# Performance work log

Hardware: AMD Instinct MI355X
Metric: run time of the kernel (lower is better)

The kernel has to match this reference:

```python
import jax, jax.numpy as jnp
import numpy as np

N = 50000
IN_CH = 128
HID = 32
HEADS = 4
OUT_CH = 64
NEG_SLOPE = 0.2


def glorot(key, shape):
    fan = shape[0] + shape[-1] if len(shape) > 1 else shape[0]
    s = jnp.sqrt(6.0 / fan)
    return jax.random.uniform(key, shape, jnp.float32, -s, s)


def setup_inputs() -> dict:
    key = jax.random.key(0)
    ks = jax.random.split(key, 10)
    x = jax.random.normal(ks[0], (N, IN_CH), jnp.float32)
    edge_index = jax.random.randint(ks[1], (2, 800000), 0, N, jnp.int32)
    return {
        "x": x,
        "edge_index": edge_index,
        # layer 1 (heads=4, concat)
        "W1": glorot(ks[2], (IN_CH, HEADS * HID)),
        "att_src1": glorot(ks[3], (HEADS, HID)),
        "att_dst1": glorot(ks[4], (HEADS, HID)),
        "b1": jnp.zeros((HEADS * HID,), jnp.float32),
        # layer 2 (heads=1, no concat)
        "W2": glorot(ks[5], (HEADS * HID, OUT_CH)),
        "att_src2": glorot(ks[6], (1, OUT_CH)),
        "att_dst2": glorot(ks[7], (1, OUT_CH)),
        "b2": jnp.zeros((OUT_CH,), jnp.float32),
    }


def gat_conv(x, src, dst, W, att_src, att_dst, b, heads, out_ch, concat):
    n = x.shape[0]
    h = (x @ W).reshape(n, heads, out_ch)                  # [N,H,C]
    a_s = jnp.einsum("nhc,hc->nh", h, att_src)            # [N,H]
    a_d = jnp.einsum("nhc,hc->nh", h, att_dst)            # [N,H]
    e = jax.nn.leaky_relu(a_s[src] + a_d[dst], NEG_SLOPE)  # [E,H]
    # segment softmax over incoming edges of each destination node
    m = jax.ops.segment_max(e, dst, num_segments=n)
    ex = jnp.exp(e - m[dst])
    denom = jax.ops.segment_sum(ex, dst, num_segments=n)
    alpha = ex / (denom[dst] + 1e-16)                      # [E,H]
    msg = h[src] * alpha[:, :, None]                       # [E,H,C]
    out = jax.ops.segment_sum(msg, dst, num_segments=n)    # [N,H,C]
    out = out.reshape(n, heads * out_ch) if concat else out.mean(axis=1)
    return out + b


def _forward(x, edge_index, W1, att_src1, att_dst1, b1, W2, att_src2, att_dst2, b2):
    n = x.shape[0]
    loop = jnp.arange(n, dtype=edge_index.dtype)
    src = jnp.concatenate([edge_index[0], loop])  # PyG adds self-loops
    dst = jnp.concatenate([edge_index[1], loop])
    h = gat_conv(x, src, dst, W1, att_src1, att_dst1, b1, HEADS, HID, True)
    h = jax.nn.relu(h)
    return gat_conv(h, src, dst, W2, att_src2, att_dst2, b2, 1, OUT_CH, False)


def reference(x, edge_index, W1, att_src1, att_dst1, b1, W2, att_src2, att_dst2, b2):
    return _forward(x, edge_index, W1, att_src1, att_dst1, b1, W2, att_src2, att_dst2, b2)
```

## Files before the change

kernel.cpp:

```cpp
#include <hip/hip_runtime.h>

#define NEG_SLOPE 0.2f

typedef unsigned int uint32;
typedef unsigned short ushort;
typedef unsigned long long u64;
typedef __fp16 f16x2 __attribute__((ext_vector_type(2)));
typedef __fp16 half8 __attribute__((ext_vector_type(8)));
typedef float f32x4 __attribute__((ext_vector_type(4)));

constexpr int IN_CH = 128;
constexpr int HID = 32;
constexpr int HEADS = 4;
constexpr int OUT_CH = 64;
constexpr int C1 = HEADS * HID;
constexpr int RB = 1024;

__device__ inline uint32 pk_f16(float lo, float hi) {
    f16x2 h = __builtin_amdgcn_cvt_pkrtz(lo, hi);
    uint32 r;
    __builtin_memcpy(&r, &h, 4);
    return r;
}
__device__ inline float f16_lo(uint32 v) {
    f16x2 h;
    __builtin_memcpy(&h, &v, 4);
    return (float)h[0];
}
__device__ inline float f16_hi(uint32 v) {
    f16x2 h;
    __builtin_memcpy(&h, &v, 4);
    return (float)h[1];
}
__device__ inline float leaky(float e) {
    return fmaxf(e, 0.f) + NEG_SLOPE * fminf(e, 0.f);
}


__global__ __launch_bounds__(256) void pack_hist_kernel(const int* __restrict__ ei, int E,
                                                        uint32* __restrict__ packed,
                                                        int* __restrict__ gcount) {
    __shared__ int lh[256];
    int t = threadIdx.x;
    lh[t] = 0;
    __syncthreads();
    int base0 = blockIdx.x * RB;
#pragma unroll
    for (int j = 0; j < 4; j++) {
        int e = base0 + j * 256 + t;
        if (e < E) {
            uint32 s = (uint32)ei[e], d = (uint32)ei[E + e];
            uint32 v = (d << 16) | s;
            packed[e] = v;
            atomicAdd(&lh[v >> 24], 1);
        }
    }
    __syncthreads();
    if (lh[t]) atomicAdd(&gcount[t], lh[t]);
}

__global__ __launch_bounds__(256) void bases_kernel(const int* __restrict__ gcount,
                                                    int* __restrict__ gbase,
                                                    int* __restrict__ cursor, int E) {
    __shared__ int cum[256];
    int t = threadIdx.x;
    int v = gcount[t];
    cum[t] = v;
    __syncthreads();
    for (int d = 1; d < 256; d <<= 1) {
        int x = (t >= d) ? cum[t - d] : 0;
        __syncthreads();
        cum[t] += x;
        __syncthreads();
    }
    int excl = cum[t] - v;
    gbase[t] = excl;
    cursor[t] = excl;
    if (t == 255) gbase[256] = E;
}

__global__ __launch_bounds__(256) void scatter_msd_kernel(const uint32* __restrict__ in,
                                                          uint32* __restrict__ out,
                                                          int* __restrict__ cursor, int E) {
    __shared__ int lcnt[256];
    __shared__ int lbase[256];
    int t = threadIdx.x;
    lcnt[t] = 0;
    __syncthreads();
    int base0 = blockIdx.x * RB;
    uint32 vals[4];
    int bks[4], rank[4];
    bool val[4];
#pragma unroll
    for (int j = 0; j < 4; j++) {
        int e = base0 + j * 256 + t;
        val[j] = e < E;
        uint32 v = val[j] ? in[e] : 0u;
        vals[j] = v;
        int b = v >> 24;
        bks[j] = b;
        if (val[j]) rank[j] = atomicAdd(&lcnt[b], 1);
    }
    __syncthreads();
    if (lcnt[t] > 0) lbase[t] = atomicAdd(&cursor[t], lcnt[t]);
    __syncthreads();
#pragma unroll
    for (int j = 0; j < 4; j++)
        if (val[j]) out[lbase[bks[j]] + rank[j]] = vals[j];
}

__global__ __launch_bounds__(256) void local_sort_kernel(const uint32* __restrict__ in,
                                                         uint32* __restrict__ out,
                                                         const int* __restrict__ gbase,
                                                         int* __restrict__ offsets, int N, int E) {
    __shared__ int hist[256];
    __shared__ int cum[256];
    int b = blockIdx.x;
    int t = threadIdx.x;
    int segstart = gbase[b];
    int segend = gbase[b + 1];
    hist[t] = 0;
    __syncthreads();
    for (int i = segstart + t; i < segend; i += 256) atomicAdd(&hist[(in[i] >> 16) & 0xff], 1);
    __syncthreads();
    int v = hist[t];
    cum[t] = v;
    __syncthreads();
    for (int d = 1; d < 256; d <<= 1) {
        int x = (t >= d) ? cum[t - d] : 0;
        __syncthreads();
        cum[t] += x;
        __syncthreads();
    }
    int myExcl = cum[t] - v;
    int dstv = b * 256 + t;
    if (dstv < N) offsets[dstv] = segstart + myExcl;
    if (b == 0 && t == 0) offsets[N] = E;
    hist[t] = myExcl;
    __syncthreads();
    for (int i = segstart + t; i < segend; i += 256) {
        uint32 w = in[i];
        int slot = atomicAdd(&hist[(w >> 16) & 0xff], 1);
        out[segstart + slot] = w;
    }
}


template <int K, int COLS, int H, bool AF16>
__global__ __launch_bounds__(256) void gemm_dots_kernel(
    const float* __restrict__ A, const float* __restrict__ W,
    const float* __restrict__ att_s, const float* __restrict__ att_d,
    uint32* __restrict__ hb, float* __restrict__ as_, float* __restrict__ ad_, int N) {
    static_assert(K == 128, "");
    constexpr int CF = COLS / 16;
    __shared__ ushort xs[64][136];
    __shared__ ushort wt[COLS][136];
    int tid = threadIdx.x;
    int row0 = blockIdx.x * 64;

#pragma unroll
    for (int l = 0; l < 4; l++) {
        int idx = tid + l * 256;
        int row = idx >> 4, kc = idx & 15;
        uint4 pkv = make_uint4(0, 0, 0, 0);
        if (row0 + row < N) {
            if constexpr (AF16) {
                pkv = *(const uint4*)((const uint32*)A + (size_t)(row0 + row) * (K / 2) + kc * 4);
            } else {
                const float* ap = A + (size_t)(row0 + row) * K + kc * 8;
                float4 v0 = *(const float4*)ap;
                float4 v1 = *(const float4*)(ap + 4);
                pkv = make_uint4(pk_f16(v0.x, v0.y), pk_f16(v0.z, v0.w), pk_f16(v1.x, v1.y),
                                 pk_f16(v1.z, v1.w));
            }
        }
        *(uint4*)&xs[row][kc * 8] = pkv;
    }
    constexpr int NP = (K / 2) * COLS / 256;
#pragma unroll
    for (int l = 0; l < NP; l++) {
        int p = tid + l * 256;
        int col = p % COLS, kp = p / COLS;
        float v0 = W[(size_t)(2 * kp) * COLS + col];
        float v1 = W[(size_t)(2 * kp + 1) * COLS + col];
        *(uint32*)&wt[col][kp * 2] = pk_f16(v0, v1);
    }
    __syncthreads();

    int w = tid >> 6, l = tid & 63;
    int q = l & 15, g = l >> 4;

    half8 af[4];
#pragma unroll
    for (int ks = 0; ks < 4; ks++) af[ks] = *(const half8*)&xs[w * 16 + q][ks * 32 + g * 8];

    f32x4 accs[CF];
#pragma unroll
    for (int cf = 0; cf < CF; cf++) {
        f32x4 a = {0.f, 0.f, 0.f, 0.f};
#pragma unroll
        for (int ks = 0; ks < 4; ks++) {
            half8 bf = *(const half8*)&wt[cf * 16 + q][ks * 32 + g * 8];
            a = __builtin_amdgcn_mfma_f32_16x16x32_f16(af[ks], bf, a, 0, 0, 0);
        }
        accs[cf] = a;
    }

    float asf[CF], adf[CF];
#pragma unroll
    for (int cf = 0; cf < CF; cf++) {
        asf[cf] = att_s[cf * 16 + q];
        adf[cf] = att_d[cf * 16 + q];
    }

#pragma unroll
    for (int r = 0; r < 4; r++) {
        int n_r = row0 + w * 16 + g * 4 + r;
        uint32 dw[CF];
        float p0 = 0.f, p1 = 0.f, p2 = 0.f, p3 = 0.f;
        float d0 = 0.f, d1 = 0.f, d2 = 0.f, d3 = 0.f;
#pragma unroll
        for (int cf = 0; cf < CF; cf++) {
            float v = accs[cf][r];
            float nb = __shfl_xor(v, 1);
            float ev = (q & 1) ? nb : v;
            float ov = (q & 1) ? v : nb;
            dw[cf] = pk_f16(ev, ov);
            float cs = v * asf[cf], cd = v * adf[cf];
            if constexpr (H == 4) {
                if (cf < 2) {
                    p0 += cs;
                    d0 += cd;
                } else if (cf < 4) {
                    p1 += cs;
                    d1 += cd;
                } else if (cf < 6) {
                    p2 += cs;
                    d2 += cd;
                } else {
                    p3 += cs;
                    d3 += cd;
                }
            } else {
                p0 += cs;
                d0 += cd;
            }
        }
#pragma unroll
        for (int dd = 1; dd < 16; dd <<= 1) {
            p0 += __shfl_xor(p0, dd);
            d0 += __shfl_xor(d0, dd);
            if constexpr (H == 4) {
                p1 += __shfl_xor(p1, dd);
                d1 += __shfl_xor(d1, dd);
                p2 += __shfl_xor(p2, dd);
                d2 += __shfl_xor(d2, dd);
                p3 += __shfl_xor(p3, dd);
                d3 += __shfl_xor(d3, dd);
            }
        }
        if (n_r < N) {
            if ((q & 1) == 0) {
                uint32* hp = hb + (size_t)n_r * (COLS / 2) + (q >> 1);
#pragma unroll
                for (int cf = 0; cf < CF; cf++) hp[cf * 8] = dw[cf];
            }
            if constexpr (H == 4) {
                if ((q >> 2) == r) {
                    int hh = q & 3;
                    float vs = hh == 0 ? p0 : hh == 1 ? p1 : hh == 2 ? p2 : p3;
                    float vd = hh == 0 ? d0 : hh == 1 ? d1 : hh == 2 ? d2 : d3;
                    as_[(size_t)n_r * 4 + hh] = vs;
                    ad_[(size_t)n_r * 4 + hh] = vd;
                }
            } else {
                if (q == r) {
                    as_[n_r] = p0;
                    ad_[n_r] = d0;
                }
            }
        }
    }
}


template <int C, int H, bool RELU, bool OUTF16>
__global__ __launch_bounds__(256) void aggregate_kernel(
    const uint32* __restrict__ hb, const float* __restrict__ as_,
    const float* __restrict__ ad_, const int* __restrict__ offsets,
    const uint32* __restrict__ csr, const float* __restrict__ bias, void* __restrict__ outp,
    int N) {
    __shared__ float plds[4][64 * H];
    __shared__ int slds[4][64];
    int gid = blockIdx.x * blockDim.x + threadIdx.x;
    int n = gid >> 6;
    int lane = threadIdx.x & 63;
    int wslot = threadIdx.x >> 6;
    if (n >= N) return;
    int off = offsets[n];
    int deg = offsets[n + 1] - off;

    float ad[H], s[H];
#pragma unroll
    for (int h = 0; h < H; h++) {
        ad[h] = ad_[(size_t)n * H + h];
        s[h] = 0.f;
    }

    constexpr int G = C / 8;
    constexpr int EPI = 64 / G;
    int eg = lane / G;
    int cl = lane % G;
    int hsel = (H == 4) ? (cl >> 2) : 0;
    float acc[8];
#pragma unroll
    for (int j = 0; j < 8; j++) acc[j] = 0.f;

    for (int base = 0; base <= deg; base += 64) {
        int my = base + lane;
        int cnt = min(64, deg + 1 - base);
        if (my <= deg) {
            int si = (my < deg) ? (int)(csr[off + my] & 0xffffu) : n;
            slds[wslot][lane] = si;
            if constexpr (H == 4) {
                float4 a = ((const float4*)as_)[si];
                float q0 = __expf(fminf(leaky(a.x + ad[0]), 80.f));
                float q1 = __expf(fminf(leaky(a.y + ad[1]), 80.f));
                float q2 = __expf(fminf(leaky(a.z + ad[2]), 80.f));
                float q3 = __expf(fminf(leaky(a.w + ad[3]), 80.f));
                s[0] += q0;
                s[1] += q1;
                s[2] += q2;
                s[3] += q3;
                ((float4*)plds[wslot])[lane] = make_float4(q0, q1, q2, q3);
            } else {
                float p = __expf(fminf(leaky(as_[si] + ad[0]), 80.f));
                s[0] += p;
                plds[wslot][lane] = p;
            }
        }
        int t2 = 0;
        for (; t2 + 2 * EPI <= cnt; t2 += 2 * EPI) {
            int tA = t2 + eg, tB = t2 + EPI + eg;
            int srcA = slds[wslot][tA];
            int srcB = slds[wslot][tB];
            float alA = plds[wslot][tA * H + hsel];
            float alB = plds[wslot][tB * H + hsel];
            uint4 uA = *(const uint4*)(hb + (size_t)srcA * (C / 2) + cl * 4);
            uint4 uB = *(const uint4*)(hb + (size_t)srcB * (C / 2) + cl * 4);
            acc[0] = fmaf(alA, f16_lo(uA.x), acc[0]);
            acc[1] = fmaf(alA, f16_hi(uA.x), acc[1]);
            acc[2] = fmaf(alA, f16_lo(uA.y), acc[2]);
            acc[3] = fmaf(alA, f16_hi(uA.y), acc[3]);
            acc[4] = fmaf(alA, f16_lo(uA.z), acc[4]);
            acc[5] = fmaf(alA, f16_hi(uA.z), acc[5]);
            acc[6] = fmaf(alA, f16_lo(uA.w), acc[6]);
            acc[7] = fmaf(alA, f16_hi(uA.w), acc[7]);
            acc[0] = fmaf(alB, f16_lo(uB.x), acc[0]);
            acc[1] = fmaf(alB, f16_hi(uB.x), acc[1]);
            acc[2] = fmaf(alB, f16_lo(uB.y), acc[2]);
            acc[3] = fmaf(alB, f16_hi(uB.y), acc[3]);
            acc[4] = fmaf(alB, f16_lo(uB.z), acc[4]);
            acc[5] = fmaf(alB, f16_hi(uB.z), acc[5]);
            acc[6] = fmaf(alB, f16_lo(uB.w), acc[6]);
            acc[7] = fmaf(alB, f16_hi(uB.w), acc[7]);
        }
        for (; t2 < cnt; t2 += EPI) {
            int te = t2 + eg;
            bool valid = te < cnt;
            int tc = valid ? te : 0;
            int src = slds[wslot][tc];
            float al = plds[wslot][tc * H + hsel];
            al = valid ? al : 0.f;
            uint4 u = *(const uint4*)(hb + (size_t)src * (C / 2) + cl * 4);
            acc[0] = fmaf(al, f16_lo(u.x), acc[0]);
            acc[1] = fmaf(al, f16_hi(u.x), acc[1]);
            acc[2] = fmaf(al, f16_lo(u.y), acc[2]);
            acc[3] = fmaf(al, f16_hi(u.y), acc[3]);
            acc[4] = fmaf(al, f16_lo(u.z), acc[4]);
            acc[5] = fmaf(al, f16_hi(u.z), acc[5]);
            acc[6] = fmaf(al, f16_lo(u.w), acc[6]);
            acc[7] = fmaf(al, f16_hi(u.w), acc[7]);
        }
    }

#pragma unroll
    for (int d = 1; d < 64; d <<= 1)
#pragma unroll
        for (int h = 0; h < H; h++) s[h] += __shfl_xor(s[h], d);
#pragma unroll
    for (int d = G; d < 64; d <<= 1)
#pragma unroll
        for (int j = 0; j < 8; j++) acc[j] += __shfl_xor(acc[j], d);

    if (eg == 0) {
        float inv = 1.f / s[hsel];
        int c = cl * 8;
        float o[8];
#pragma unroll
        for (int j = 0; j < 8; j++) {
            o[j] = fmaf(acc[j], inv, bias[c + j]);
            if (RELU) o[j] = fmaxf(o[j], 0.f);
        }
        if constexpr (OUTF16) {
            uint4 pkv = make_uint4(pk_f16(o[0], o[1]), pk_f16(o[2], o[3]), pk_f16(o[4], o[5]),
                                   pk_f16(o[6], o[7]));
            *(uint4*)((uint32*)outp + (size_t)n * (C / 2) + cl * 4) = pkv;
        } else {
            float* out = (float*)outp;
            *(float4*)(out + (size_t)n * C + c) = make_float4(o[0], o[1], o[2], o[3]);
            *(float4*)(out + (size_t)n * C + c + 4) = make_float4(o[4], o[5], o[6], o[7]);
        }
    }
}


extern "C" void kernel_launch(void* const* d_in, const int* in_sizes, int n_in,
                              void* d_out, int out_size, void* d_ws, size_t ws_size,
                              hipStream_t stream) {
    const float* x = (const float*)d_in[0];
    const int* ei = (const int*)d_in[1];
    const float* W1 = (const float*)d_in[2];
    const float* att_src1 = (const float*)d_in[3];
    const float* att_dst1 = (const float*)d_in[4];
    const float* b1 = (const float*)d_in[5];
    const float* W2 = (const float*)d_in[6];
    const float* att_src2 = (const float*)d_in[7];
    const float* att_dst2 = (const float*)d_in[8];
    const float* b2 = (const float*)d_in[9];

    int N = in_sizes[0] / IN_CH;
    int E = in_sizes[1] / 2;

    char* wsp = (char*)d_ws;
    size_t off = 0;
    auto carve = [&](size_t bytes) -> void* {
        void* p = wsp + off;
        off = (off + bytes + 255) & ~(size_t)255;
        return p;
    };
    int nblocks = (E + RB - 1) / RB;

    uint32* packed = (uint32*)carve((size_t)E * 4);
    uint32* tmp = (uint32*)carve((size_t)E * 4);
    int* gcount = (int*)carve(1024);
    int* gbase = (int*)carve(1032);
    int* cursor = (int*)carve(1024);
    int* offsets = (int*)carve((size_t)(N + 1) * 4);
    uint32* h1b = (uint32*)carve((size_t)N * C1 * 2);
    uint32* h2b = (uint32*)carve((size_t)N * OUT_CH * 2);
    uint32* out1h = (uint32*)carve((size_t)N * C1 * 2);
    float* as1 = (float*)carve((size_t)N * HEADS * 4);
    float* ad1 = (float*)carve((size_t)N * HEADS * 4);
    float* as2 = (float*)carve((size_t)N * 4);
    float* ad2 = (float*)carve((size_t)N * 4);

    int nbuckets = (N + 255) / 256;
    hipMemsetAsync(gcount, 0, 1024, stream);
    pack_hist_kernel<<<nblocks, 256, 0, stream>>>(ei, E, packed, gcount);
    bases_kernel<<<1, 256, 0, stream>>>(gcount, gbase, cursor, E);
    scatter_msd_kernel<<<nblocks, 256, 0, stream>>>(packed, tmp, cursor, E);
    local_sort_kernel<<<nbuckets, 256, 0, stream>>>(tmp, packed, gbase, offsets, N, E);

    int nwaveblocks = (N * 64 + 255) / 256;
    int ngemmblocks = (N + 63) / 64;

    gemm_dots_kernel<128, 128, 4, false>
        <<<ngemmblocks, 256, 0, stream>>>(x, W1, att_src1, att_dst1, h1b, as1, ad1, N);
    aggregate_kernel<128, 4, true, true>
        <<<nwaveblocks, 256, 0, stream>>>(h1b, as1, ad1, offsets, packed, b1, (void*)out1h, N);

    gemm_dots_kernel<128, 64, 1, true><<<ngemmblocks, 256, 0, stream>>>(
        (const float*)out1h, W2, att_src2, att_dst2, h2b, as2, ad2, N);
    aggregate_kernel<64, 1, false, false>
        <<<nwaveblocks, 256, 0, stream>>>(h2b, as2, ad2, offsets, packed, b2, d_out, N);
}
```

Measured before the change: 153.4 us.

## Replace global atomic cursors with per-block histogram scan; remap aggregate blocks across XCDs

```diff
diff --git a/kernel.cpp b/kernel.cpp
--- a/kernel.cpp
+++ b/kernel.cpp
@@ -39,7 +39,7 @@
 
 __global__ __launch_bounds__(256) void pack_hist_kernel(const int* __restrict__ ei, int E,
                                                         uint32* __restrict__ packed,
-                                                        int* __restrict__ gcount) {
+                                                        int* __restrict__ ghist, int nblocks) {
     __shared__ int lh[256];
     int t = threadIdx.x;
     lh[t] = 0;
@@ -56,15 +56,46 @@
         }
     }
     __syncthreads();
-    if (lh[t]) atomicAdd(&gcount[t], lh[t]);
-}
-
-__global__ __launch_bounds__(256) void bases_kernel(const int* __restrict__ gcount,
-                                                    int* __restrict__ gbase,
-                                                    int* __restrict__ cursor, int E) {
+    ghist[(size_t)t * nblocks + blockIdx.x] = lh[t];
+}
+
+__global__ __launch_bounds__(256) void rowscan_kernel(int* __restrict__ ghist,
+                                                      int* __restrict__ totals, int nblocks) {
+    __shared__ int ts[256];
+    int b = blockIdx.x, t = threadIdx.x;
+    int per = (nblocks + 255) >> 8;
+    int* row = ghist + (size_t)b * nblocks;
+    int v[8];
+    int s = 0;
+#pragma unroll
+    for (int i = 0; i < 8; i++) {
+        int idx = t * per + i;
+        v[i] = (i < per && idx < nblocks) ? row[idx] : 0;
+        s += v[i];
+    }
+    ts[t] = s;
+    __syncthreads();
+    for (int d = 1; d < 256; d <<= 1) {
+        int x = (t >= d) ? ts[t - d] : 0;
+        __syncthreads();
+        ts[t] += x;
+        __syncthreads();
+    }
+    int ex = (t > 0) ? ts[t - 1] : 0;
+    if (t == 255) totals[b] = ts[255];
+#pragma unroll
+    for (int i = 0; i < 8; i++) {
+        int idx = t * per + i;
+        if (i < per && idx < nblocks) row[idx] = ex;
+        ex += v[i];
+    }
+}
+
+__global__ __launch_bounds__(256) void bases_kernel(const int* __restrict__ totals,
+                                                    int* __restrict__ gbase, int E) {
     __shared__ int cum[256];
     int t = threadIdx.x;
-    int v = gcount[t];
+    int v = totals[t];
     cum[t] = v;
     __syncthreads();
     for (int d = 1; d < 256; d <<= 1) {
@@ -73,40 +104,29 @@
         cum[t] += x;
         __syncthreads();
     }
-    int excl = cum[t] - v;
-    gbase[t] = excl;
-    cursor[t] = excl;
+    gbase[t] = cum[t] - v;
     if (t == 255) gbase[256] = E;
 }
 
 __global__ __launch_bounds__(256) void scatter_msd_kernel(const uint32* __restrict__ in,
                                                           uint32* __restrict__ out,
-                                                          int* __restrict__ cursor, int E) {
-    __shared__ int lcnt[256];
+                                                          const int* __restrict__ ghist,
+                                                          const int* __restrict__ gbase, int E,
+                                                          int nblocks) {
     __shared__ int lbase[256];
     int t = threadIdx.x;
-    lcnt[t] = 0;
+    lbase[t] = ghist[(size_t)t * nblocks + blockIdx.x] + gbase[t];
     __syncthreads();
     int base0 = blockIdx.x * RB;
-    uint32 vals[4];
-    int bks[4], rank[4];
-    bool val[4];
 #pragma unroll
     for (int j = 0; j < 4; j++) {
         int e = base0 + j * 256 + t;
-        val[j] = e < E;
-        uint32 v = val[j] ? in[e] : 0u;
-        vals[j] = v;
-        int b = v >> 24;
-        bks[j] = b;
-        if (val[j]) rank[j] = atomicAdd(&lcnt[b], 1);
-    }
-    __syncthreads();
-    if (lcnt[t] > 0) lbase[t] = atomicAdd(&cursor[t], lcnt[t]);
-    __syncthreads();
-#pragma unroll
-    for (int j = 0; j < 4; j++)
-        if (val[j]) out[lbase[bks[j]] + rank[j]] = vals[j];
+        if (e < E) {
+            uint32 v = in[e];
+            int slot = atomicAdd(&lbase[v >> 24], 1);
+            out[slot] = v;
+        }
+    }
 }
 
 __global__ __launch_bounds__(256) void local_sort_kernel(const uint32* __restrict__ in,
@@ -292,10 +312,14 @@
     int N) {
     __shared__ float plds[4][64 * H];
     __shared__ int slds[4][64];
-    int gid = blockIdx.x * blockDim.x + threadIdx.x;
-    int n = gid >> 6;
+    int bid = blockIdx.x;
+    int nwg = gridDim.x;
+    int qq = nwg >> 3, rr = nwg & 7;
+    int xcd = bid & 7, jj = bid >> 3;
+    int work = (xcd < rr ? xcd * (qq + 1) : rr * (qq + 1) + (xcd - rr) * qq) + jj;
     int lane = threadIdx.x & 63;
     int wslot = threadIdx.x >> 6;
+    int n = work * 4 + wslot;
     if (n >= N) return;
     int off = offsets[n];
     int deg = offsets[n + 1] - off;
@@ -440,12 +464,13 @@
         return p;
     };
     int nblocks = (E + RB - 1) / RB;
+    int L = 256 * nblocks;
 
     uint32* packed = (uint32*)carve((size_t)E * 4);
     uint32* tmp = (uint32*)carve((size_t)E * 4);
-    int* gcount = (int*)carve(1024);
+    int* ghist = (int*)carve((size_t)L * 4);
+    int* totals = (int*)carve(1024);
     int* gbase = (int*)carve(1032);
-    int* cursor = (int*)carve(1024);
     int* offsets = (int*)carve((size_t)(N + 1) * 4);
     uint32* h1b = (uint32*)carve((size_t)N * C1 * 2);
     uint32* h2b = (uint32*)carve((size_t)N * OUT_CH * 2);
@@ -455,12 +480,11 @@
     float* as2 = (float*)carve((size_t)N * 4);
     float* ad2 = (float*)carve((size_t)N * 4);
 
-    int nbuckets = (N + 255) / 256;
-    hipMemsetAsync(gcount, 0, 1024, stream);
-    pack_hist_kernel<<<nblocks, 256, 0, stream>>>(ei, E, packed, gcount);
-    bases_kernel<<<1, 256, 0, stream>>>(gcount, gbase, cursor, E);
-    scatter_msd_kernel<<<nblocks, 256, 0, stream>>>(packed, tmp, cursor, E);
-    local_sort_kernel<<<nbuckets, 256, 0, stream>>>(tmp, packed, gbase, offsets, N, E);
+    pack_hist_kernel<<<nblocks, 256, 0, stream>>>(ei, E, packed, ghist, nblocks);
+    rowscan_kernel<<<256, 256, 0, stream>>>(ghist, totals, nblocks);
+    bases_kernel<<<1, 256, 0, stream>>>(totals, gbase, E);
+    scatter_msd_kernel<<<nblocks, 256, 0, stream>>>(packed, tmp, ghist, gbase, E, nblocks);
+    local_sort_kernel<<<(N + 255) / 256, 256, 0, stream>>>(tmp, packed, gbase, offsets, N, E);
 
     int nwaveblocks = (N * 64 + 255) / 256;
     int ngemmblocks = (N + 63) / 64;
```

New measurement: 126.7 us. 1.21x faster.
